# Kernel tuning notes

Hardware: AMD Instinct MI355X
Metric: run time of the kernel (lower is better)

The kernel has to match this reference:

```python
import jax, jax.numpy as jnp
import numpy as np

N = 100000
IN_C = 128
OUT_C = 32
HEADS = 4
E = 1600000
NEG_SLOPE = 0.2


def setup_inputs() -> dict:
    key = jax.random.key(0)
    ks = jax.random.split(key, 8)
    x = jax.random.normal(ks[0], (N, IN_C), dtype=jnp.float32)
    edge_index = jax.random.randint(ks[1], (2, E), 0, N, dtype=jnp.int64)
    # GATConv params (PyG conventions): lin weight [H*C, in], att vectors [H, C], bias [H*C]
    sc = 1.0 / np.sqrt(IN_C)
    W = jax.random.uniform(ks[2], (HEADS * OUT_C, IN_C), dtype=jnp.float32, minval=-sc, maxval=sc)
    att_src = jax.random.normal(ks[3], (HEADS, OUT_C), dtype=jnp.float32) * 0.1
    att_dst = jax.random.normal(ks[4], (HEADS, OUT_C), dtype=jnp.float32) * 0.1
    bias_conv = jnp.zeros((HEADS * OUT_C,), dtype=jnp.float32)
    # final nn.Linear(H*C, C)
    sl = 1.0 / np.sqrt(HEADS * OUT_C)
    W_lin = jax.random.uniform(ks[5], (OUT_C, HEADS * OUT_C), dtype=jnp.float32, minval=-sl, maxval=sl)
    b_lin = jax.random.uniform(ks[6], (OUT_C,), dtype=jnp.float32, minval=-sl, maxval=sl)
    return {"x": x, "edge_index": edge_index, "W": W, "att_src": att_src,
            "att_dst": att_dst, "bias_conv": bias_conv, "W_lin": W_lin, "b_lin": b_lin}


def reference(x, edge_index, W, att_src, att_dst, bias_conv, W_lin, b_lin):
    n = x.shape[0]
    # add self loops (PyG default)
    loops = jnp.arange(n, dtype=edge_index.dtype)
    src = jnp.concatenate([edge_index[0], loops])
    dst = jnp.concatenate([edge_index[1], loops])
    # linear projection, per-head split: [N, H, C]
    h = (x @ W.T).reshape(n, HEADS, OUT_C)
    # per-node attention logits
    a_src = jnp.einsum('nhc,hc->nh', h, att_src)  # [N, H]
    a_dst = jnp.einsum('nhc,hc->nh', h, att_dst)  # [N, H]
    e = a_src[src] + a_dst[dst]                   # [E', H]
    e = jax.nn.leaky_relu(e, NEG_SLOPE)
    # segment softmax over incoming edges per destination node
    m = jax.ops.segment_max(e, dst, num_segments=n)       # [N, H]
    e = jnp.exp(e - m[dst])
    s = jax.ops.segment_sum(e, dst, num_segments=n)       # [N, H]
    alpha = e / s[dst]                                    # [E', H]
    # scatter-aggregate alpha-weighted source features
    msg = alpha[:, :, None] * h[src]                      # [E', H, C]
    out = jax.ops.segment_sum(msg, dst, num_segments=n)   # [N, H, C]
    out = out.reshape(n, HEADS * OUT_C) + bias_conv
    # final linear + ELU
    return jax.nn.elu(out @ W_lin.T + b_lin)
```

## Files before the change

### kernel.cpp

```cpp
#include <hip/hip_runtime.h>
#include <hip/hip_fp16.h>
#include <cstdint>
#include <cstddef>

#define NHEADS 4
#define OUT_C 32
#define HC 128
#define IN_CH 128
#define NEG_SLOPE 0.2f
#define LDSPAD 136
#define KEDGE 4096

typedef _Float16 half8 __attribute__((ext_vector_type(8)));
typedef float floatx4 __attribute__((ext_vector_type(4)));

static inline size_t align256(size_t v) { return (v + 255) & ~(size_t)255; }

__device__ __forceinline__ float lrelu(float v) { return v > 0.f ? v : NEG_SLOPE * v; }

__device__ __forceinline__ float wred_sum(float v) {
    v += __shfl_xor(v, 1);
    v += __shfl_xor(v, 2);
    v += __shfl_xor(v, 4);
    v += __shfl_xor(v, 8);
    v += __shfl_xor(v, 16);
    v += __shfl_xor(v, 32);
    return v;
}

__device__ __forceinline__ unsigned int pack_h2(float a, float b) {
    __half2 h = __floats2half2_rn(a, b);
    return *reinterpret_cast<unsigned int*>(&h);
}
__device__ __forceinline__ float2 unpack_h2(unsigned int u) {
    __half2 h = *reinterpret_cast<__half2*>(&u);
    return __half22float2(h);
}

__device__ __forceinline__ int detect_f64(const int* __restrict__ ei, int E, int* sf) {
    int t = threadIdx.x;
    if (t == 0) *sf = 0;
    __syncthreads();
    int lim = E < 1024 ? E : 1024;
    int acc = 0;
    for (int i = t; i < lim; i += 256) acc |= ei[2 * i + 1];
    acc |= __shfl_xor(acc, 1);
    acc |= __shfl_xor(acc, 2);
    acc |= __shfl_xor(acc, 4);
    acc |= __shfl_xor(acc, 8);
    acc |= __shfl_xor(acc, 16);
    acc |= __shfl_xor(acc, 32);
    if ((t & 63) == 0 && acc) atomicOr(sf, 1);
    __syncthreads();
    return *sf == 0;
}

__global__ __launch_bounds__(256) void gemm_hist(const float* __restrict__ x,
                                                 const float* __restrict__ W,
                                                 const float* __restrict__ att_src,
                                                 const float* __restrict__ att_dst,
                                                 __half* __restrict__ h,
                                                 float* __restrict__ a_src,
                                                 float* __restrict__ a_dst, int n,
                                                 const int* __restrict__ ei,
                                                 int* __restrict__ bcount,
                                                 int E, int sh, int GB) {
    __shared__ __align__(16) _Float16 Ws[128 * LDSPAD];
    __shared__ __align__(16) _Float16 Xs[128 * LDSPAD];
    __shared__ int hc[256];
    __shared__ int sf;
    int tid = threadIdx.x;

    if (blockIdx.x >= GB) {
        hc[tid] = 0;
        int f64 = detect_f64(ei, E, &sf);
        int nbh = gridDim.x - GB;
        int stride = nbh * 256;
        for (int i = (blockIdx.x - GB) * 256 + tid; i < E; i += stride) {
            int d;
            if (f64) d = (int)((const long long*)ei)[(size_t)E + i];
            else     d = ei[(size_t)E + i];
            atomicAdd(&hc[d >> sh], 1);
        }
        __syncthreads();
        if (hc[tid]) atomicAdd(&bcount[tid], hc[tid]);
        return;
    }
    int rowbase = blockIdx.x << 7;

    const float4* wf = (const float4*)W;
#pragma unroll
    for (int i = 0; i < 16; ++i) {
        int u = (i << 8) + tid;
        int r = u >> 5, g = u & 31;
        float4 v = wf[u];
        uint2 uu;
        uu.x = pack_h2(v.x, v.y);
        uu.y = pack_h2(v.z, v.w);
        *(uint2*)&Ws[r * LDSPAD + (g << 2)] = uu;
    }
    const float4* x4 = (const float4*)x;
#pragma unroll
    for (int i = 0; i < 16; ++i) {
        int u = (i << 8) + tid;
        int r = u >> 5, c4 = u & 31;
        int row = rowbase + r;
        if (row >= n) row = n - 1;
        float4 v = x4[((size_t)row << 5) + c4];
        uint2 uu;
        uu.x = pack_h2(v.x, v.y);
        uu.y = pack_h2(v.z, v.w);
        *(uint2*)&Xs[r * LDSPAD + (c4 << 2)] = uu;
    }
    __syncthreads();

    int lane = tid & 63, w = tid >> 6;
    int quad = lane >> 4, Lm = lane & 15;
    floatx4 acc[2][8];
#pragma unroll
    for (int rt = 0; rt < 2; ++rt)
#pragma unroll
        for (int c = 0; c < 8; ++c) acc[rt][c] = (floatx4){0.f, 0.f, 0.f, 0.f};

#pragma unroll
    for (int kc = 0; kc < 128; kc += 32) {
        int ko = kc + (quad << 3);
        half8 a0 = *(const half8*)&Xs[((w << 5) + Lm) * LDSPAD + ko];
        half8 a1 = *(const half8*)&Xs[((w << 5) + 16 + Lm) * LDSPAD + ko];
#pragma unroll
        for (int c = 0; c < 8; ++c) {
            half8 b = *(const half8*)&Ws[((c << 4) + Lm) * LDSPAD + ko];
            acc[0][c] = __builtin_amdgcn_mfma_f32_16x16x32_f16(a0, b, acc[0][c], 0, 0, 0);
            acc[1][c] = __builtin_amdgcn_mfma_f32_16x16x32_f16(a1, b, acc[1][c], 0, 0, 0);
        }
    }
    __syncthreads();
#pragma unroll
    for (int rt = 0; rt < 2; ++rt)
#pragma unroll
        for (int c = 0; c < 8; ++c)
#pragma unroll
            for (int i = 0; i < 4; ++i) {
                int rl = (w << 5) + (rt << 4) + (quad << 2) + i;
                int cl = (c << 4) + Lm;
                Xs[rl * LDSPAD + cl] = (_Float16)acc[rt][c][i];
            }
    __syncthreads();
#pragma unroll
    for (int i = 0; i < 8; ++i) {
        int u = (i << 8) + tid;
        int r = u >> 4, g = u & 15;
        int row = rowbase + r;
        if (row < n) {
            uint4 v = *(uint4*)&Xs[r * LDSPAD + (g << 3)];
            *(uint4*)(h + ((size_t)row << 7) + (g << 3)) = v;
        }
    }
    int r = tid >> 1, seg = tid & 1;
    int row = rowbase + r;
    const _Float16* hp = &Xs[r * LDSPAD + (seg << 6)];
    float sa = 0.f, da = 0.f, sb = 0.f, db = 0.f;
#pragma unroll
    for (int g8 = 0; g8 < 8; ++g8) {
        half8 v = *(const half8*)&hp[g8 << 3];
        int co = (seg << 6) + (g8 << 3);
        float4 A1 = *(const float4*)&att_src[co];
        float4 A2 = *(const float4*)&att_src[co + 4];
        float4 D1 = *(const float4*)&att_dst[co];
        float4 D2 = *(const float4*)&att_dst[co + 4];
        float f0 = (float)v[0], f1 = (float)v[1], f2 = (float)v[2], f3 = (float)v[3];
        float f4 = (float)v[4], f5 = (float)v[5], f6 = (float)v[6], f7 = (float)v[7];
        float ts = f0 * A1.x + f1 * A1.y + f2 * A1.z + f3 * A1.w
                 + f4 * A2.x + f5 * A2.y + f6 * A2.z + f7 * A2.w;
        float td = f0 * D1.x + f1 * D1.y + f2 * D1.z + f3 * D1.w
                 + f4 * D2.x + f5 * D2.y + f6 * D2.z + f7 * D2.w;
        if (g8 < 4) { sa += ts; da += td; } else { sb += ts; db += td; }
    }
    if (row < n) {
        int base = (row << 2) + (seg << 1);
        a_src[base] = sa;
        a_src[base + 1] = sb;
        a_dst[base] = da;
        a_dst[base + 1] = db;
    }
}

__global__ __launch_bounds__(256) void bscatter(const int* __restrict__ ei,
                                                const int* __restrict__ bcount,
                                                int* __restrict__ gcursor,
                                                int2* __restrict__ bkt,
                                                int E, int n, int sh) {
    __shared__ int cnt[256], base[256], lcur[256], ts[256];
    __shared__ int sf;
    int t = threadIdx.x;
    cnt[t] = 0;
    lcur[t] = 0;
    int f64 = detect_f64(ei, E, &sf);
    int total = E + n;
    int i0 = blockIdx.x * KEDGE;
    int ed[16], es[16];
#pragma unroll
    for (int j = 0; j < 16; ++j) {
        int i = i0 + (j << 8) + t;
        int s = 0, d = -1;
        if (i < total) {
            if (i < E) {
                if (f64) {
                    s = (int)((const long long*)ei)[i];
                    d = (int)((const long long*)ei)[(size_t)E + i];
                } else {
                    s = ei[i];
                    d = ei[(size_t)E + i];
                }
            } else {
                s = d = i - E;
            }
            atomicAdd(&cnt[d >> sh], 1);
        }
        ed[j] = d;
        es[j] = s;
    }
    int lo = t << sh, hi = (t + 1) << sh;
    if (hi > n) hi = n;
    int nodes = hi > lo ? hi - lo : 0;
    int v = bcount[t] + nodes;
    ts[t] = v;
    __syncthreads();
    int run = v;
    for (int d = 1; d < 256; d <<= 1) {
        int o = (t >= d) ? ts[t - d] : 0;
        __syncthreads();
        run += o;
        ts[t] = run;
        __syncthreads();
    }
    int excl = run - v;
    base[t] = excl + (cnt[t] ? atomicAdd(&gcursor[t], cnt[t]) : 0);
    __syncthreads();
#pragma unroll
    for (int j = 0; j < 16; ++j) {
        int d = ed[j];
        if (d >= 0) {
            int b = d >> sh;
            int pos = base[b] + atomicAdd(&lcur[b], 1);
            bkt[pos] = make_int2(d, es[j]);
        }
    }
}

__global__ __launch_bounds__(256) void bsort(const int2* __restrict__ bkt,
                                             const int* __restrict__ bcount,
                                             const float* __restrict__ a_src,
                                             const float* __restrict__ a_dst,
                                             int* __restrict__ off,
                                             int4* __restrict__ recs,
                                             int n, int E, int sh) {
    __shared__ int cnt[512], offl[512], ts[256];
    __shared__ __align__(16) float sad[512 * 4];
    int t = threadIdx.x, bid = blockIdx.x;
    int lo = t << sh, hi = (t + 1) << sh;
    if (hi > n) hi = n;
    int nodes = hi > lo ? hi - lo : 0;
    int v = bcount[t] + nodes;
    ts[t] = v;
    __syncthreads();
    int run = v;
    for (int d = 1; d < 256; d <<= 1) {
        int o = (t >= d) ? ts[t - d] : 0;
        __syncthreads();
        run += o;
        ts[t] = run;
        __syncthreads();
    }
    int e0 = (bid > 0) ? ts[bid - 1] : 0;
    int e1 = ts[bid];
    if (bid == gridDim.x - 1 && t == 0) off[n] = E + n;
    int node0 = bid << sh;
    int node1 = (bid + 1) << sh;
    if (node1 > n) node1 = n;
    int nn = node1 - node0;
    __syncthreads();
    cnt[t] = 0;
    cnt[t + 256] = 0;
    const float4* ad4 = (const float4*)a_dst;
    for (int i = t; i < nn; i += 256)
        *(float4*)&sad[i << 2] = ad4[node0 + i];
    __syncthreads();
    for (int i = e0 + t; i < e1; i += 256) {
        int2 e = bkt[i];
        atomicAdd(&cnt[e.x - node0], 1);
    }
    __syncthreads();
    int a = cnt[t << 1], b = cnt[(t << 1) + 1];
    int s = a + b;
    ts[t] = s;
    __syncthreads();
    run = s;
    for (int d = 1; d < 256; d <<= 1) {
        int o = (t >= d) ? ts[t - d] : 0;
        __syncthreads();
        run += o;
        ts[t] = run;
        __syncthreads();
    }
    int excl = run - s;
    offl[t << 1] = excl;
    offl[(t << 1) + 1] = excl + a;
    cnt[t << 1] = 0;
    cnt[(t << 1) + 1] = 0;
    __syncthreads();
    for (int i = t; i < nn; i += 256) off[node0 + i] = e0 + offl[i];
    const float4* as4 = (const float4*)a_src;
    for (int i = e0 + t; i < e1; i += 256) {
        int2 e = bkt[i];
        int li = e.x - node0;
        float4 as = as4[e.y];
        float4 ad = *(const float4*)&sad[li << 2];
        int4 rec;
        rec.x = e.y;
        rec.y = (int)pack_h2(__expf(lrelu(as.x + ad.x)), __expf(lrelu(as.y + ad.y)));
        rec.z = (int)pack_h2(__expf(lrelu(as.z + ad.z)), __expf(lrelu(as.w + ad.w)));
        rec.w = 0;
        int pos = e0 + offl[li] + atomicAdd(&cnt[li], 1);
        recs[pos] = rec;
    }
}

__device__ __forceinline__ void accum_half(const int* ssrc, const float* sal,
                                           const __half* __restrict__ h,
                                           int deg, int half, int L, int head,
                                           float4& acc) {
    float4 a0 = {0, 0, 0, 0}, a1 = {0, 0, 0, 0}, a2 = {0, 0, 0, 0}, a3 = {0, 0, 0, 0};
    int j = half;
    for (; j + 14 < deg; j += 16) {
        int s0 = ssrc[j], s1 = ssrc[j + 2], s2 = ssrc[j + 4], s3 = ssrc[j + 6];
        int s4 = ssrc[j + 8], s5 = ssrc[j + 10], s6 = ssrc[j + 12], s7 = ssrc[j + 14];
        float w0 = sal[(j << 2) + head];
        float w1 = sal[((j + 2) << 2) + head];
        float w2 = sal[((j + 4) << 2) + head];
        float w3 = sal[((j + 6) << 2) + head];
        float w4 = sal[((j + 8) << 2) + head];
        float w5 = sal[((j + 10) << 2) + head];
        float w6 = sal[((j + 12) << 2) + head];
        float w7 = sal[((j + 14) << 2) + head];
        uint2 u0 = *(const uint2*)(h + ((size_t)s0 << 7) + (L << 2));
        uint2 u1 = *(const uint2*)(h + ((size_t)s1 << 7) + (L << 2));
        uint2 u2 = *(const uint2*)(h + ((size_t)s2 << 7) + (L << 2));
        uint2 u3 = *(const uint2*)(h + ((size_t)s3 << 7) + (L << 2));
        uint2 u4 = *(const uint2*)(h + ((size_t)s4 << 7) + (L << 2));
        uint2 u5 = *(const uint2*)(h + ((size_t)s5 << 7) + (L << 2));
        uint2 u6 = *(const uint2*)(h + ((size_t)s6 << 7) + (L << 2));
        uint2 u7 = *(const uint2*)(h + ((size_t)s7 << 7) + (L << 2));
        float2 fa, fb;
        fa = unpack_h2(u0.x); fb = unpack_h2(u0.y);
        a0.x = fmaf(w0, fa.x, a0.x); a0.y = fmaf(w0, fa.y, a0.y);
        a0.z = fmaf(w0, fb.x, a0.z); a0.w = fmaf(w0, fb.y, a0.w);
        fa = unpack_h2(u1.x); fb = unpack_h2(u1.y);
        a1.x = fmaf(w1, fa.x, a1.x); a1.y = fmaf(w1, fa.y, a1.y);
        a1.z = fmaf(w1, fb.x, a1.z); a1.w = fmaf(w1, fb.y, a1.w);
        fa = unpack_h2(u2.x); fb = unpack_h2(u2.y);
        a2.x = fmaf(w2, fa.x, a2.x); a2.y = fmaf(w2, fa.y, a2.y);
        a2.z = fmaf(w2, fb.x, a2.z); a2.w = fmaf(w2, fb.y, a2.w);
        fa = unpack_h2(u3.x); fb = unpack_h2(u3.y);
        a3.x = fmaf(w3, fa.x, a3.x); a3.y = fmaf(w3, fa.y, a3.y);
        a3.z = fmaf(w3, fb.x, a3.z); a3.w = fmaf(w3, fb.y, a3.w);
        fa = unpack_h2(u4.x); fb = unpack_h2(u4.y);
        a0.x = fmaf(w4, fa.x, a0.x); a0.y = fmaf(w4, fa.y, a0.y);
        a0.z = fmaf(w4, fb.x, a0.z); a0.w = fmaf(w4, fb.y, a0.w);
        fa = unpack_h2(u5.x); fb = unpack_h2(u5.y);
        a1.x = fmaf(w5, fa.x, a1.x); a1.y = fmaf(w5, fa.y, a1.y);
        a1.z = fmaf(w5, fb.x, a1.z); a1.w = fmaf(w5, fb.y, a1.w);
        fa = unpack_h2(u6.x); fb = unpack_h2(u6.y);
        a2.x = fmaf(w6, fa.x, a2.x); a2.y = fmaf(w6, fa.y, a2.y);
        a2.z = fmaf(w6, fb.x, a2.z); a2.w = fmaf(w6, fb.y, a2.w);
        fa = unpack_h2(u7.x); fb = unpack_h2(u7.y);
        a3.x = fmaf(w7, fa.x, a3.x); a3.y = fmaf(w7, fa.y, a3.y);
        a3.z = fmaf(w7, fb.x, a3.z); a3.w = fmaf(w7, fb.y, a3.w);
    }
    for (; j + 6 < deg; j += 8) {
        int s0 = ssrc[j], s1 = ssrc[j + 2], s2 = ssrc[j + 4], s3 = ssrc[j + 6];
        float w0 = sal[(j << 2) + head];
        float w1 = sal[((j + 2) << 2) + head];
        float w2 = sal[((j + 4) << 2) + head];
        float w3 = sal[((j + 6) << 2) + head];
        uint2 u0 = *(const uint2*)(h + ((size_t)s0 << 7) + (L << 2));
        uint2 u1 = *(const uint2*)(h + ((size_t)s1 << 7) + (L << 2));
        uint2 u2 = *(const uint2*)(h + ((size_t)s2 << 7) + (L << 2));
        uint2 u3 = *(const uint2*)(h + ((size_t)s3 << 7) + (L << 2));
        float2 fa, fb;
        fa = unpack_h2(u0.x); fb = unpack_h2(u0.y);
        a0.x = fmaf(w0, fa.x, a0.x); a0.y = fmaf(w0, fa.y, a0.y);
        a0.z = fmaf(w0, fb.x, a0.z); a0.w = fmaf(w0, fb.y, a0.w);
        fa = unpack_h2(u1.x); fb = unpack_h2(u1.y);
        a1.x = fmaf(w1, fa.x, a1.x); a1.y = fmaf(w1, fa.y, a1.y);
        a1.z = fmaf(w1, fb.x, a1.z); a1.w = fmaf(w1, fb.y, a1.w);
        fa = unpack_h2(u2.x); fb = unpack_h2(u2.y);
        a2.x = fmaf(w2, fa.x, a2.x); a2.y = fmaf(w2, fa.y, a2.y);
        a2.z = fmaf(w2, fb.x, a2.z); a2.w = fmaf(w2, fb.y, a2.w);
        fa = unpack_h2(u3.x); fb = unpack_h2(u3.y);
        a3.x = fmaf(w3, fa.x, a3.x); a3.y = fmaf(w3, fa.y, a3.y);
        a3.z = fmaf(w3, fb.x, a3.z); a3.w = fmaf(w3, fb.y, a3.w);
    }
    for (; j < deg; j += 2) {
        int s0 = ssrc[j];
        float w0 = sal[(j << 2) + head];
        uint2 u0 = *(const uint2*)(h + ((size_t)s0 << 7) + (L << 2));
        float2 fa = unpack_h2(u0.x), fb = unpack_h2(u0.y);
        a0.x = fmaf(w0, fa.x, a0.x); a0.y = fmaf(w0, fa.y, a0.y);
        a0.z = fmaf(w0, fb.x, a0.z); a0.w = fmaf(w0, fb.y, a0.w);
    }
    acc.x += (a0.x + a1.x) + (a2.x + a3.x);
    acc.y += (a0.y + a1.y) + (a2.y + a3.y);
    acc.z += (a0.z + a1.z) + (a2.z + a3.z);
    acc.w += (a0.w + a1.w) + (a2.w + a3.w);
}

__global__ __launch_bounds__(256) void aggregate(const __half* __restrict__ h,
                                                 const int4* __restrict__ recs,
                                                 const int* __restrict__ off,
                                                 const float* __restrict__ bias,
                                                 __half* __restrict__ agg, int n) {
    __shared__ __align__(16) int sh_src[4][64];
    __shared__ __align__(16) float sh_al[4][256];
    int wslot = threadIdx.x >> 6;
    int lane = threadIdx.x & 63;
    int wid = blockIdx.x * 4 + wslot;
    int nw = gridDim.x * 4;
    int L = lane & 31, half = lane >> 5, head = L >> 3;
    float4 b4 = ((const float4*)bias)[L];
    int* ssrc = sh_src[wslot];
    float* sal = sh_al[wslot];

    for (int node = wid; node < n; node += nw) {
        int start = off[node], end = off[node + 1];
        int deg = end - start;
        float4 acc = {0.f, 0.f, 0.f, 0.f};
        float4 psum = {0.f, 0.f, 0.f, 0.f};

        if (deg <= 64) {
            bool v = lane < deg;
            int idx = start + (v ? lane : 0);
            int4 rec = recs[idx];
            float2 pa = unpack_h2((unsigned)rec.y);
            float2 pb = unpack_h2((unsigned)rec.z);
            float4 p = {pa.x, pa.y, pb.x, pb.y};
            if (!v) p = make_float4(0.f, 0.f, 0.f, 0.f);
            psum = p;
            ssrc[lane] = rec.x;
            *(float4*)&sal[lane << 2] = p;
            asm volatile("s_waitcnt lgkmcnt(0)" ::: "memory");
            accum_half(ssrc, sal, h, deg, half, L, head, acc);
            asm volatile("" ::: "memory");
        } else {
            for (int bb = 0; bb < deg; bb += 64) {
                int i = bb + lane;
                bool v = i < deg;
                int idx = start + (v ? i : 0);
                int4 rec = recs[idx];
                float2 pa = unpack_h2((unsigned)rec.y);
                float2 pb = unpack_h2((unsigned)rec.z);
                float4 p = {pa.x, pa.y, pb.x, pb.y};
                if (!v) p = make_float4(0.f, 0.f, 0.f, 0.f);
                psum.x += p.x; psum.y += p.y; psum.z += p.z; psum.w += p.w;
                ssrc[lane] = rec.x;
                *(float4*)&sal[lane << 2] = p;
                asm volatile("s_waitcnt lgkmcnt(0)" ::: "memory");
                int cl = deg - bb;
                if (cl > 64) cl = 64;
                accum_half(ssrc, sal, h, cl, half, L, head, acc);
                asm volatile("" ::: "memory");
            }
        }
        float s0 = wred_sum(psum.x), s1 = wred_sum(psum.y);
        float s2 = wred_sum(psum.z), s3 = wred_sum(psum.w);
        float sh = (head == 0) ? s0 : (head == 1) ? s1 : (head == 2) ? s2 : s3;
        float inv = 1.f / sh;
        acc.x += __shfl_xor(acc.x, 32);
        acc.y += __shfl_xor(acc.y, 32);
        acc.z += __shfl_xor(acc.z, 32);
        acc.w += __shfl_xor(acc.w, 32);
        if (lane < 32) {
            float4 res = {fmaf(acc.x, inv, b4.x), fmaf(acc.y, inv, b4.y),
                          fmaf(acc.z, inv, b4.z), fmaf(acc.w, inv, b4.w)};
            uint2 u;
            u.x = pack_h2(res.x, res.y);
            u.y = pack_h2(res.z, res.w);
            *(uint2*)(agg + ((size_t)node << 7) + (L << 2)) = u;
        }
    }
}

__global__ __launch_bounds__(256) void proj(const __half* __restrict__ agg,
                                            const float* __restrict__ W_lin,
                                            const float* __restrict__ b_lin,
                                            float* __restrict__ out, int n) {
    __shared__ float xs[64][132];
    __shared__ float wt[128][36];
    int tid = threadIdx.x;
    const float4* w4 = (const float4*)W_lin;
#pragma unroll
    for (int i = 0; i < 4; ++i) {
        int f4 = (i << 8) + tid;
        int o = f4 >> 5, kk = (f4 & 31) << 2;
        float4 w = w4[f4];
        wt[kk][o] = w.x;
        wt[kk + 1][o] = w.y;
        wt[kk + 2][o] = w.z;
        wt[kk + 3][o] = w.w;
    }
    int rowbase = blockIdx.x << 6;
    const uint4* a4 = (const uint4*)agg;
#pragma unroll
    for (int i = 0; i < 4; ++i) {
        int f8 = (i << 8) + tid;
        int r = f8 >> 4, cc = (f8 & 15) << 3;
        int row = rowbase + r;
        if (row >= n) row = n - 1;
        uint4 u = a4[((size_t)row << 4) + (cc >> 3)];
        float2 f0 = unpack_h2(u.x), f1 = unpack_h2(u.y);
        float2 f2 = unpack_h2(u.z), f3 = unpack_h2(u.w);
        float* xp = &xs[r][cc];
        xp[0] = f0.x; xp[1] = f0.y; xp[2] = f1.x; xp[3] = f1.y;
        xp[4] = f2.x; xp[5] = f2.y; xp[6] = f3.x; xp[7] = f3.y;
    }
    __syncthreads();
    int r = tid >> 2, cg = tid & 3, c0 = cg << 3;
    float acc[8];
#pragma unroll
    for (int j = 0; j < 8; ++j) acc[j] = 0.f;
    for (int k = 0; k < 128; k += 4) {
        float4 xv = *(const float4*)&xs[r][k];
        float xk[4] = {xv.x, xv.y, xv.z, xv.w};
#pragma unroll
        for (int kk = 0; kk < 4; ++kk) {
            float4 wa = *(const float4*)&wt[k + kk][c0];
            float4 wb = *(const float4*)&wt[k + kk][c0 + 4];
            acc[0] = fmaf(xk[kk], wa.x, acc[0]);
            acc[1] = fmaf(xk[kk], wa.y, acc[1]);
            acc[2] = fmaf(xk[kk], wa.z, acc[2]);
            acc[3] = fmaf(xk[kk], wa.w, acc[3]);
            acc[4] = fmaf(xk[kk], wb.x, acc[4]);
            acc[5] = fmaf(xk[kk], wb.y, acc[5]);
            acc[6] = fmaf(xk[kk], wb.z, acc[6]);
            acc[7] = fmaf(xk[kk], wb.w, acc[7]);
        }
    }
    int row = rowbase + r;
    if (row < n) {
        float res[8];
#pragma unroll
        for (int j = 0; j < 8; ++j) {
            float v = acc[j] + b_lin[c0 + j];
            res[j] = v > 0.f ? v : (__expf(v) - 1.f);
        }
        float4* op = (float4*)(out + (size_t)row * 32 + c0);
        op[0] = make_float4(res[0], res[1], res[2], res[3]);
        op[1] = make_float4(res[4], res[5], res[6], res[7]);
    }
}

extern "C" void kernel_launch(void* const* d_in, const int* in_sizes, int n_in,
                              void* d_out, int out_size, void* d_ws, size_t ws_size,
                              hipStream_t stream) {
    const float* x = (const float*)d_in[0];
    const int* ei = (const int*)d_in[1];
    const float* W = (const float*)d_in[2];
    const float* att_src = (const float*)d_in[3];
    const float* att_dst = (const float*)d_in[4];
    const float* bias_conv = (const float*)d_in[5];
    const float* W_lin = (const float*)d_in[6];
    const float* b_lin = (const float*)d_in[7];
    int n = in_sizes[0] / IN_CH;
    int E = in_sizes[1] / 2;

    int sh = 0;
    while (((n + (1 << sh) - 1) >> sh) > 256) sh++;
    int NB = (n + (1 << sh) - 1) >> sh;

    char* ws = (char*)d_ws;
    size_t o = 0;
    auto alloc = [&](size_t bytes) { char* p = ws + o; o = align256(o + bytes); return p; };
    __half* h      = (__half*)alloc((size_t)n * HC * 2);
    __half* agg    = (__half*)alloc((size_t)n * HC * 2);
    float* a_src   = (float*)alloc((size_t)n * NHEADS * 4);
    float* a_dst   = (float*)alloc((size_t)n * NHEADS * 4);
    int* off       = (int*)alloc(((size_t)n + 1) * 4);
    int* bcount    = (int*)alloc(256 * 4);
    int* gcursor   = (int*)alloc(256 * 4);
    int4* recs     = (int4*)alloc((size_t)(E + n + 64) * 16);
    int2* bkt      = (int2*)alloc((size_t)(E + n + 64) * 8);

    hipMemsetAsync(bcount, 0, 2048, stream);

    int GB = (n + 127) / 128;
    int NBH = 1024;
    gemm_hist<<<GB + NBH, 256, 0, stream>>>(x, W, att_src, att_dst, h, a_src, a_dst, n,
                                            ei, bcount, E, sh, GB);
    bscatter<<<(E + n + KEDGE - 1) / KEDGE, 256, 0, stream>>>(ei, bcount, gcursor, bkt, E, n, sh);
    bsort<<<NB, 256, 0, stream>>>(bkt, bcount, a_src, a_dst, off, recs, n, E, sh);
    aggregate<<<2048, 256, 0, stream>>>(h, recs, off, bias_conv, agg, n);
    proj<<<(n + 63) / 64, 256, 0, stream>>>(agg, W_lin, b_lin, (float*)d_out, n);
}
```

Measured before the change: 307.0 us.

## Compute edge attention weights during bucket scatter instead of in bucket sort

The per-edge exp(leaky_relu(a_src+a_dst)) computation moves from the per-bucket sort kernel into the scatter kernel. The scatter now writes 16-byte records carrying dst, src and packed half weights, and the sort only permutes them. Scatter blocks also halve their edge count to raise block-level parallelism for the extra gather work. The cost is that the bucket buffer doubles in size, which adds write and read traffic, and the scatter loses the LDS-cached a_dst and instead gathers both a_src and a_dst randomly from global memory.

```diff
diff --git a/kernel.cpp b/kernel.cpp
--- a/kernel.cpp
+++ b/kernel.cpp
@@ -9,7 +9,7 @@
 #define IN_CH 128
 #define NEG_SLOPE 0.2f
 #define LDSPAD 136
-#define KEDGE 4096
+#define KEDGE 2048
 
 typedef _Float16 half8 __attribute__((ext_vector_type(8)));
 typedef float floatx4 __attribute__((ext_vector_type(4)));
@@ -188,7 +188,9 @@
 __global__ __launch_bounds__(256) void bscatter(const int* __restrict__ ei,
                                                 const int* __restrict__ bcount,
                                                 int* __restrict__ gcursor,
-                                                int2* __restrict__ bkt,
+                                                const float* __restrict__ a_src,
+                                                const float* __restrict__ a_dst,
+                                                int4* __restrict__ bkt,
                                                 int E, int n, int sh) {
     __shared__ int cnt[256], base[256], lcur[256], ts[256];
     __shared__ int sf;
@@ -198,9 +200,9 @@
     int f64 = detect_f64(ei, E, &sf);
     int total = E + n;
     int i0 = blockIdx.x * KEDGE;
-    int ed[16], es[16];
-#pragma unroll
-    for (int j = 0; j < 16; ++j) {
+    int ed[8], es[8];
+#pragma unroll
+    for (int j = 0; j < 8; ++j) {
         int i = i0 + (j << 8) + t;
         int s = 0, d = -1;
         if (i < total) {
@@ -237,26 +239,33 @@
     int excl = run - v;
     base[t] = excl + (cnt[t] ? atomicAdd(&gcursor[t], cnt[t]) : 0);
     __syncthreads();
-#pragma unroll
-    for (int j = 0; j < 16; ++j) {
+    const float4* as4 = (const float4*)a_src;
+    const float4* ad4 = (const float4*)a_dst;
+#pragma unroll
+    for (int j = 0; j < 8; ++j) {
         int d = ed[j];
         if (d >= 0) {
+            int s = es[j];
+            float4 as = as4[s];
+            float4 ad = ad4[d];
+            int4 rec;
+            rec.x = d;
+            rec.y = s;
+            rec.z = (int)pack_h2(__expf(lrelu(as.x + ad.x)), __expf(lrelu(as.y + ad.y)));
+            rec.w = (int)pack_h2(__expf(lrelu(as.z + ad.z)), __expf(lrelu(as.w + ad.w)));
             int b = d >> sh;
             int pos = base[b] + atomicAdd(&lcur[b], 1);
-            bkt[pos] = make_int2(d, es[j]);
-        }
-    }
-}
-
-__global__ __launch_bounds__(256) void bsort(const int2* __restrict__ bkt,
+            bkt[pos] = rec;
+        }
+    }
+}
+
+__global__ __launch_bounds__(256) void bsort(const int4* __restrict__ bkt,
                                              const int* __restrict__ bcount,
-                                             const float* __restrict__ a_src,
-                                             const float* __restrict__ a_dst,
                                              int* __restrict__ off,
                                              int4* __restrict__ recs,
                                              int n, int E, int sh) {
     __shared__ int cnt[512], offl[512], ts[256];
-    __shared__ __align__(16) float sad[512 * 4];
     int t = threadIdx.x, bid = blockIdx.x;
     int lo = t << sh, hi = (t + 1) << sh;
     if (hi > n) hi = n;
@@ -282,13 +291,9 @@
     __syncthreads();
     cnt[t] = 0;
     cnt[t + 256] = 0;
-    const float4* ad4 = (const float4*)a_dst;
-    for (int i = t; i < nn; i += 256)
-        *(float4*)&sad[i << 2] = ad4[node0 + i];
     __syncthreads();
     for (int i = e0 + t; i < e1; i += 256) {
-        int2 e = bkt[i];
-        atomicAdd(&cnt[e.x - node0], 1);
+        atomicAdd(&cnt[bkt[i].x - node0], 1);
     }
     __syncthreads();
     int a = cnt[t << 1], b = cnt[(t << 1) + 1];
@@ -310,19 +315,11 @@
     cnt[(t << 1) + 1] = 0;
     __syncthreads();
     for (int i = t; i < nn; i += 256) off[node0 + i] = e0 + offl[i];
-    const float4* as4 = (const float4*)a_src;
     for (int i = e0 + t; i < e1; i += 256) {
-        int2 e = bkt[i];
+        int4 e = bkt[i];
         int li = e.x - node0;
-        float4 as = as4[e.y];
-        float4 ad = *(const float4*)&sad[li << 2];
-        int4 rec;
-        rec.x = e.y;
-        rec.y = (int)pack_h2(__expf(lrelu(as.x + ad.x)), __expf(lrelu(as.y + ad.y)));
-        rec.z = (int)pack_h2(__expf(lrelu(as.z + ad.z)), __expf(lrelu(as.w + ad.w)));
-        rec.w = 0;
         int pos = e0 + offl[li] + atomicAdd(&cnt[li], 1);
-        recs[pos] = rec;
+        recs[pos] = make_int4(e.y, e.z, e.w, 0);
     }
 }
 
@@ -588,7 +585,7 @@
     int* bcount    = (int*)alloc(256 * 4);
     int* gcursor   = (int*)alloc(256 * 4);
     int4* recs     = (int4*)alloc((size_t)(E + n + 64) * 16);
-    int2* bkt      = (int2*)alloc((size_t)(E + n + 64) * 8);
+    int4* bkt      = (int4*)alloc((size_t)(E + n + 64) * 16);
 
     hipMemsetAsync(bcount, 0, 2048, stream);
 
@@ -596,8 +593,9 @@
     int NBH = 1024;
     gemm_hist<<<GB + NBH, 256, 0, stream>>>(x, W, att_src, att_dst, h, a_src, a_dst, n,
                                             ei, bcount, E, sh, GB);
-    bscatter<<<(E + n + KEDGE - 1) / KEDGE, 256, 0, stream>>>(ei, bcount, gcursor, bkt, E, n, sh);
-    bsort<<<NB, 256, 0, stream>>>(bkt, bcount, a_src, a_dst, off, recs, n, E, sh);
+    bscatter<<<(E + n + KEDGE - 1) / KEDGE, 256, 0, stream>>>(ei, bcount, gcursor,
+                                                              a_src, a_dst, bkt, E, n, sh);
+    bsort<<<NB, 256, 0, stream>>>(bkt, bcount, off, recs, n, E, sh);
     aggregate<<<2048, 256, 0, stream>>>(h, recs, off, bias_conv, agg, n);
     proj<<<(n + 63) / 64, 256, 0, stream>>>(agg, W_lin, b_lin, (float*)d_out, n);
 }
```

Result: slower. 330.1 us (+7.5%).
